# Kernel optimization log

Hardware: AMD Instinct MI355X
Metric: run time of the kernel (lower is better)

## Reference

```python
import jax, jax.numpy as jnp
import numpy as np

LEAKY_SLOPE = 0.01
BN_EPS = 1e-5


def _local_conv(x, w, b, stride):
    # x: [B,C,H,W]; w: [1,O,C,OH,OW,K] (K = kh*kw, kh==kw); b: [1,O,OH,OW]
    sh, sw = stride
    _, O, C, oh, ow, K = w.shape
    k = int(round(K ** 0.5))
    # gather unfold patches: torch .unfold(2,kh,dh).unfold(3,kw,dw) -> last dim ordered (i major, j minor)
    patches = jnp.stack(
        [x[:, :, i:i + sh * oh:sh, j:j + sw * ow:sw] for i in range(k) for j in range(k)],
        axis=-1)  # [B,C,oh,ow,K]
    out = jnp.einsum('bchwk,ochwk->bohw', patches, w[0])
    return out + b  # b broadcasts [1,O,OH,OW]


def _bn_train(x, gamma, beta):
    # BatchNorm2d in training mode: biased batch statistics over (N,H,W)
    m = jnp.mean(x, axis=(0, 2, 3), keepdims=True)
    v = jnp.var(x, axis=(0, 2, 3), keepdims=True)
    return gamma[None, :, None, None] * (x - m) * jax.lax.rsqrt(v + BN_EPS) + beta[None, :, None, None]


def _lrelu(x):
    return jnp.where(x >= 0, x, LEAKY_SLOPE * x)


def _pad1(x):
    return jnp.pad(x, ((0, 0), (0, 0), (1, 1), (1, 1)))


def setup_inputs() -> dict:
    key = jax.random.key(0)
    ks = jax.random.split(key, 16)
    B = 8192
    inp = {
        'image': jax.random.normal(ks[0], (B, 10, 9, 1), jnp.float32),
        'conv1_w': jax.random.normal(ks[1], (64, 1, 2, 2), jnp.float32) * 0.5,
        'conv1_b': jax.random.normal(ks[2], (64,), jnp.float32) * 0.1,
        'lc1_w': jax.random.normal(ks[3], (1, 16, 64, 10, 5, 9), jnp.float32) * 0.05,
        'lc1_b': jax.random.normal(ks[4], (1, 16, 10, 5), jnp.float32) * 0.1,
        'lc2_w': jax.random.normal(ks[5], (1, 8, 16, 11, 6, 4), jnp.float32) * 0.1,
        'lc2_b': jax.random.normal(ks[6], (1, 8, 11, 6), jnp.float32) * 0.1,
        'lc3_w': jax.random.normal(ks[7], (1, 8, 8, 12, 4, 4), jnp.float32) * 0.1,
        'lc3_b': jax.random.normal(ks[8], (1, 8, 12, 4), jnp.float32) * 0.1,
        'gamma1': jax.random.normal(ks[9], (16,), jnp.float32) * 0.1 + 1.0,
        'beta1': jax.random.normal(ks[10], (16,), jnp.float32) * 0.1,
        'gamma2': jax.random.normal(ks[11], (8,), jnp.float32) * 0.1 + 1.0,
        'beta2': jax.random.normal(ks[12], (8,), jnp.float32) * 0.1,
        'gamma3': jax.random.normal(ks[13], (8,), jnp.float32) * 0.1 + 1.0,
        'beta3': jax.random.normal(ks[14], (8,), jnp.float32) * 0.1,
    }
    return inp


def reference(image, conv1_w, conv1_b, lc1_w, lc1_b, lc2_w, lc2_b, lc3_w, lc3_b,
              gamma1, beta1, gamma2, beta2, gamma3, beta3):
    x = jnp.transpose(image, (0, 3, 1, 2))  # [B,1,10,9]
    # Conv2d kernel 2, padding='same' (torch pads extra on right/bottom for even kernels)
    x = jax.lax.conv_general_dilated(
        x, conv1_w, window_strides=(1, 1), padding=[(0, 1), (0, 1)],
        dimension_numbers=('NCHW', 'OIHW', 'NCHW'))
    x = x + conv1_b[None, :, None, None]
    x = _lrelu(x)
    x = _pad1(x)                               # [B,64,12,11]
    x = _local_conv(x, lc1_w, lc1_b, (1, 2))   # [B,16,10,5]
    x = _lrelu(x)
    x = _bn_train(x, gamma1, beta1)
    x = _pad1(x)                               # [B,16,12,7]
    x = _local_conv(x, lc2_w, lc2_b, (1, 1))   # [B,8,11,6]
    x = _lrelu(x)
    x = _bn_train(x, gamma2, beta2)
    x = _pad1(x)                               # [B,8,13,8]
    x = _local_conv(x, lc3_w, lc3_b, (1, 2))   # [B,8,12,4]
    x = _lrelu(x)
    x = _bn_train(x, gamma3, beta3)
    return x.reshape(x.shape[0], -1)           # [B,384]
```

## Files before the change

### kernel.cpp

```cpp
#include <hip/hip_runtime.h>


typedef float  f32x4 __attribute__((ext_vector_type(4)));
typedef float  f32x2 __attribute__((ext_vector_type(2)));
typedef short  bf16x8 __attribute__((ext_vector_type(8)));

union FR  { int4 i4; bf16x8 bf; unsigned u[4]; };

#define LRELU(v) fmaxf((v), 0.01f * (v))

static __device__ inline unsigned bfr(float f) {
    unsigned u = __float_as_uint(f);
    return (u + 0x7fffu + ((u >> 16) & 1u)) >> 16;
}
static __device__ inline unsigned short bfr16(float f) { return (unsigned short)bfr(f); }
static __device__ inline float ubf(unsigned lo16) { return __uint_as_float(lo16 << 16); }

#if __has_builtin(__builtin_elementwise_fma)
static __device__ inline f32x2 pk_fma(f32x2 a, f32x2 b, f32x2 c) { return __builtin_elementwise_fma(a, b, c); }
#else
static __device__ inline f32x2 pk_fma(f32x2 a, f32x2 b, f32x2 c) { return a * b + c; }
#endif
static __device__ inline f32x2 pk_lrelu(f32x2 v) {
#if __has_builtin(__builtin_elementwise_max)
    return __builtin_elementwise_max(v, v * 0.01f);
#else
    f32x2 r; r.x = LRELU(v.x); r.y = LRELU(v.y); return r;
#endif
}
static __device__ inline float aload(float* p) {
    return __hip_atomic_load(p, __ATOMIC_RELAXED, __HIP_MEMORY_SCOPE_AGENT);
}

union PrepSM { float imgP[16][110]; float wt[9216]; };

__global__ __launch_bounds__(256) void kprep(
    const float* __restrict__ imgp,
    const float* __restrict__ cw,
    const float* __restrict__ cb,
    const float* __restrict__ lw1,
    unsigned* __restrict__ x1u,
    int4* __restrict__ afg1, float* __restrict__ stats,
    int nA, int doAux, int spp)
{
    __shared__ PrepSM sm;
    const int bx = blockIdx.x, tid = threadIdx.x;

    if (bx < nA) {
        const int sb = bx * 16;
        for (int e = tid; e < 1760; e += 256) ((float*)sm.imgP)[e] = 0.0f;
        __syncthreads();
        for (int e = tid; e < 1440; e += 256) {
            int s = e / 90, hw = e - s * 90;
            int r = hw / 9, c = hw - r * 9;
            sm.imgP[s][r * 10 + c] = imgp[(size_t)sb * 90 + e];
        }
        __syncthreads();

        const int chp = tid & 31, sidx = tid >> 5;
        const int ch0 = 2 * chp;
        const int h = chp >> 4, chpos = chp & 15;
        f32x2 w00 = {cw[ch0 * 4 + 0], cw[ch0 * 4 + 4]};
        f32x2 w01 = {cw[ch0 * 4 + 1], cw[ch0 * 4 + 5]};
        f32x2 w10 = {cw[ch0 * 4 + 2], cw[ch0 * 4 + 6]};
        f32x2 w11 = {cw[ch0 * 4 + 3], cw[ch0 * 4 + 7]};
        f32x2 bb  = {cb[ch0], cb[ch0 + 1]};

        #pragma unroll
        for (int ss = 0; ss < 2; ++ss) {
            const int s = sidx + 8 * ss;
            const float* ip = sm.imgP[s];
            unsigned* dst = x1u + ((size_t)h * spp + (sb + s)) * 16 + chpos;
            #pragma unroll 2
            for (int r = 0; r < 10; ++r) {
                #pragma unroll
                for (int c = 0; c < 9; ++c) {
                    f32x2 v = bb;
                    v = pk_fma((f32x2)ip[r * 10 + c],      w00, v);
                    v = pk_fma((f32x2)ip[r * 10 + c + 1],  w01, v);
                    v = pk_fma((f32x2)ip[r * 10 + c + 10], w10, v);
                    v = pk_fma((f32x2)ip[r * 10 + c + 11], w11, v);
                    v = pk_lrelu(v);
                    dst[(size_t)(r * 9 + c) * 2 * spp * 16] = bfr(v.x) | (bfr(v.y) << 16);
                }
            }
        }
        return;
    }
    if (!doAux) return;

    const int b2 = bx - nA;
    if (b2 < 50) {
        const int pos = b2;
        for (int e = tid; e < 9216; e += 256) {
            int pair = e / 9, t = e - 9 * pair;
            sm.wt[e] = lw1[pair * 450 + pos * 9 + t];
        }
        __syncthreads();
        for (int e = tid; e < 1152; e += 256) {
            int l = e & 63, ht = e >> 6;
            int h = (ht >= 9) ? 1 : 0, t = ht - 9 * h;
            int q = l >> 4, o = l & 15;
            unsigned uu[4];
            #pragma unroll
            for (int p = 0; p < 4; ++p) {
                int c0 = 32 * h + 8 * q + 2 * p;
                float a0 = sm.wt[(o * 64 + c0) * 9 + t];
                float a1 = sm.wt[(o * 64 + c0 + 1) * 9 + t];
                uu[p] = bfr(a0) | (bfr(a1) << 16);
            }
            int4 st = { (int)uu[0], (int)uu[1], (int)uu[2], (int)uu[3] };
            afg1[pos * 1152 + e] = st;
        }
    } else if (tid < 64) stats[tid] = 0.0f;
}

__global__ __launch_bounds__(256) void k1_lc1(
    const int4* __restrict__ x1v,
    const int4* __restrict__ afg,
    const float* __restrict__ lb,
    unsigned short* __restrict__ y1b,
    float* __restrict__ stats,
    int sampOff, int spp, int nc)
{
    __shared__ int4  AfL[1152];
    __shared__ float bl[16];
    __shared__ float red[32];

    int pos, chunk;
    {
        int id = blockIdx.x;
        if (nc >= 8) { int k8 = id & 7; int r = id >> 3; pos = r % 50; chunk = (r / 50) * 8 + k8; }
        else         { pos = id % 50; chunk = id / 50; }
    }
    const int oh = pos / 5, ow = pos % 5;
    const int tid = threadIdx.x;
    const int wv = tid >> 6, lane = tid & 63;
    const int lane15 = lane & 15, q = lane >> 4;

    for (int e = tid; e < 1152; e += 256) AfL[e] = afg[pos * 1152 + e];
    if (tid < 16) bl[tid] = lb[tid * 50 + pos];
    if (tid < 32) red[tid] = 0.0f;
    __syncthreads();

    const int sLoc = chunk * 256 + wv * 64;
    const int sAbs = sampOff + sLoc;
    const int spp4 = spp * 4;

    int base_g[4];
    #pragma unroll
    for (int g = 0; g < 4; ++g)
        base_g[g] = (sLoc + g * 16 + lane15) * 4 + q;

    f32x4 acc[4];
    #pragma unroll
    for (int g = 0; g < 4; ++g) acc[g] = (f32x4){0.f, 0.f, 0.f, 0.f};

    #pragma unroll
    for (int t = 0; t < 9; ++t) {
        const int ti = t / 3, tj = t % 3;
        const int r = oh + ti - 1, c2 = 2 * ow + tj - 1;
        if (r >= 0 && r < 10 && c2 >= 0 && c2 < 9) {
            const int hw = r * 9 + c2;
            #pragma unroll
            for (int h = 0; h < 2; ++h) {
                FR fa; fa.i4 = AfL[(h * 9 + t) * 64 + lane];
                const int slabBase = (hw * 2 + h) * spp4;
                #pragma unroll
                for (int g = 0; g < 4; ++g) {
                    FR fb; fb.i4 = x1v[slabBase + base_g[g]];
                    acc[g] = __builtin_amdgcn_mfma_f32_16x16x32_bf16(fa.bf, fb.bf, acc[g], 0, 0, 0);
                }
            }
        }
    }

    float so[4] = {0, 0, 0, 0}, sq[4] = {0, 0, 0, 0};
    #pragma unroll
    for (int g = 0; g < 4; ++g)
        #pragma unroll
        for (int r = 0; r < 4; ++r) {
            int o = q * 4 + r;
            float v = acc[g][r] + bl[o];
            v = LRELU(v);
            y1b[(size_t)(o * 50 + pos) * 8192 + sAbs + g * 16 + lane15] = bfr16(v);
            so[r] += v; sq[r] += v * v;
        }
    #pragma unroll
    for (int r = 0; r < 4; ++r) {
        #pragma unroll
        for (int m = 1; m < 16; m <<= 1) {
            so[r] += __shfl_xor(so[r], m, 16);
            sq[r] += __shfl_xor(sq[r], m, 16);
        }
        if (lane15 == 0) {
            int o = q * 4 + r;
            atomicAdd(&red[o], so[r]);
            atomicAdd(&red[16 + o], sq[r]);
        }
    }
    __syncthreads();
    if (tid < 32) atomicAdd(&stats[tid], red[tid]);
}

__global__ __launch_bounds__(256) void k2_lc2(
    const unsigned short* __restrict__ y1b,
    const float* __restrict__ lw2, const float* __restrict__ lb2,
    const float* __restrict__ g1, const float* __restrict__ be1,
    unsigned short* __restrict__ y2b, float* __restrict__ stats)
{
    __shared__ float wld[512];
    __shared__ float a1[16], b1[16], bl[8], red[16];

    const int unit = blockIdx.x;
    const int pos = unit >> 3, chunk = unit & 7;
    const int oh = pos / 6, ow = pos % 6;
    const int tid = threadIdx.x, lane = tid & 63;

    if (tid < 128) {
        const float* src = lw2 + tid * 264 + pos * 4;
        int o = tid >> 4, c = tid & 15;
        #pragma unroll
        for (int k = 0; k < 4; k++) wld[c * 32 + k * 8 + o] = src[k];
    }
    if (tid < 16) {
        float m = aload(&stats[tid]) * (1.0f / 409600.0f);
        float v = aload(&stats[16 + tid]) * (1.0f / 409600.0f) - m * m;
        float a = g1[tid] * rsqrtf(v + 1e-5f);
        a1[tid] = a; b1[tid] = be1[tid] - a * m;
        if (tid < 8) bl[tid] = lb2[tid * 66 + pos];
        red[tid] = 0.0f;
    }
    __syncthreads();

    int base[4]; float kmv[4];
    #pragma unroll
    for (int i = 0; i < 2; i++)
        #pragma unroll
        for (int j = 0; j < 2; j++) {
            int r = oh + i - 1, c2 = ow + j - 1;
            bool ok = (r >= 0 && r < 10 && c2 >= 0 && c2 < 5);
            int rc = min(max(r, 0), 9), cc2 = min(max(c2, 0), 4);
            base[i * 2 + j] = rc * 5 + cc2;
            kmv[i * 2 + j] = ok ? 1.0f : 0.0f;
        }

    const int sb = chunk * 1024 + tid * 4;
    float acc[8][4];
    #pragma unroll
    for (int o = 0; o < 8; o++)
        #pragma unroll
        for (int s = 0; s < 4; s++) acc[o][s] = bl[o];

    #pragma unroll 1
    for (int c = 0; c < 16; c++) {
        float av = a1[c], bv = b1[c];
        float p[4][4];
        #pragma unroll
        for (int t = 0; t < 4; t++) {
            float ap = av * kmv[t], bp = bv * kmv[t];
            uint2 U = *(const uint2*)(y1b + (size_t)(c * 50 + base[t]) * 8192 + sb);
            p[t][0] = fmaf(ap, ubf(U.x & 0xffffu), bp);
            p[t][1] = fmaf(ap, __uint_as_float(U.x & 0xffff0000u), bp);
            p[t][2] = fmaf(ap, ubf(U.y & 0xffffu), bp);
            p[t][3] = fmaf(ap, __uint_as_float(U.y & 0xffff0000u), bp);
        }
        const float4* wr = (const float4*)&wld[c * 32];
        #pragma unroll
        for (int t = 0; t < 4; t++) {
            float4 wa = wr[t * 2], wb = wr[t * 2 + 1];
            #pragma unroll
            for (int s = 0; s < 4; s++) {
                float pv = p[t][s];
                acc[0][s] += wa.x * pv; acc[1][s] += wa.y * pv;
                acc[2][s] += wa.z * pv; acc[3][s] += wa.w * pv;
                acc[4][s] += wb.x * pv; acc[5][s] += wb.y * pv;
                acc[6][s] += wb.z * pv; acc[7][s] += wb.w * pv;
            }
        }
    }

    #pragma unroll
    for (int o = 0; o < 8; o++) {
        float v0 = LRELU(acc[o][0]), v1 = LRELU(acc[o][1]);
        float v2 = LRELU(acc[o][2]), v3 = LRELU(acc[o][3]);
        uint2 st = { bfr(v0) | (bfr(v1) << 16), bfr(v2) | (bfr(v3) << 16) };
        *(uint2*)(y2b + (size_t)(o * 66 + pos) * 8192 + sb) = st;
        float sv = v0 + v1 + v2 + v3;
        float sqv = v0 * v0 + v1 * v1 + v2 * v2 + v3 * v3;
        #pragma unroll
        for (int m = 32; m > 0; m >>= 1) {
            sv  += __shfl_xor(sv, m, 64);
            sqv += __shfl_xor(sqv, m, 64);
        }
        if (lane == 0) { atomicAdd(&red[o], sv); atomicAdd(&red[8 + o], sqv); }
    }
    __syncthreads();
    if (tid < 16) atomicAdd(&stats[32 + tid], red[tid]);
}

__global__ __launch_bounds__(256) void k3_lc3(
    const unsigned short* __restrict__ y2b,
    const float* __restrict__ lw3, const float* __restrict__ lb3,
    const float* __restrict__ g2, const float* __restrict__ be2,
    unsigned short* __restrict__ y3b, float* __restrict__ stats)
{
    __shared__ float wld[256];
    __shared__ float a2[8], b2[8], bl[8], red[16];

    const int unit = blockIdx.x;
    const int pos = unit >> 3, chunk = unit & 7;
    const int oh = pos >> 2, ow = pos & 3;
    const int tid = threadIdx.x, lane = tid & 63;

    if (tid < 64) {
        const float* src = lw3 + tid * 192 + pos * 4;
        int o = tid >> 3, c = tid & 7;
        #pragma unroll
        for (int k = 0; k < 4; k++) wld[c * 32 + k * 8 + o] = src[k];
    }
    if (tid < 16) {
        if (tid < 8) {
            float m = aload(&stats[32 + tid]) * (1.0f / 540672.0f);
            float v = aload(&stats[40 + tid]) * (1.0f / 540672.0f) - m * m;
            float a = g2[tid] * rsqrtf(v + 1e-5f);
            a2[tid] = a; b2[tid] = be2[tid] - a * m;
            bl[tid] = lb3[tid * 48 + pos];
        }
        red[tid] = 0.0f;
    }
    __syncthreads();

    int base[4]; float kmv[4];
    #pragma unroll
    for (int i = 0; i < 2; i++)
        #pragma unroll
        for (int j = 0; j < 2; j++) {
            int r = oh + i - 1, c2 = 2 * ow + j - 1;
            bool ok = (r >= 0 && r < 11 && c2 >= 0 && c2 < 6);
            int rc = min(max(r, 0), 10), cc2 = min(max(c2, 0), 5);
            base[i * 2 + j] = rc * 6 + cc2;
            kmv[i * 2 + j] = ok ? 1.0f : 0.0f;
        }

    const int sb = chunk * 1024 + tid * 4;
    float acc[8][4];
    #pragma unroll
    for (int o = 0; o < 8; o++)
        #pragma unroll
        for (int s = 0; s < 4; s++) acc[o][s] = bl[o];

    #pragma unroll 1
    for (int c = 0; c < 8; c++) {
        float av = a2[c], bv = b2[c];
        float p[4][4];
        #pragma unroll
        for (int t = 0; t < 4; t++) {
            float ap = av * kmv[t], bp = bv * kmv[t];
            uint2 U = *(const uint2*)(y2b + (size_t)(c * 66 + base[t]) * 8192 + sb);
            p[t][0] = fmaf(ap, ubf(U.x & 0xffffu), bp);
            p[t][1] = fmaf(ap, __uint_as_float(U.x & 0xffff0000u), bp);
            p[t][2] = fmaf(ap, ubf(U.y & 0xffffu), bp);
            p[t][3] = fmaf(ap, __uint_as_float(U.y & 0xffff0000u), bp);
        }
        const float4* wr = (const float4*)&wld[c * 32];
        #pragma unroll
        for (int t = 0; t < 4; t++) {
            float4 wa = wr[t * 2], wb = wr[t * 2 + 1];
            #pragma unroll
            for (int s = 0; s < 4; s++) {
                float pv = p[t][s];
                acc[0][s] += wa.x * pv; acc[1][s] += wa.y * pv;
                acc[2][s] += wa.z * pv; acc[3][s] += wa.w * pv;
                acc[4][s] += wb.x * pv; acc[5][s] += wb.y * pv;
                acc[6][s] += wb.z * pv; acc[7][s] += wb.w * pv;
            }
        }
    }

    #pragma unroll
    for (int o = 0; o < 8; o++) {
        float v0 = LRELU(acc[o][0]), v1 = LRELU(acc[o][1]);
        float v2 = LRELU(acc[o][2]), v3 = LRELU(acc[o][3]);
        uint2 st = { bfr(v0) | (bfr(v1) << 16), bfr(v2) | (bfr(v3) << 16) };
        *(uint2*)(y3b + (size_t)(o * 48 + pos) * 8192 + sb) = st;
        float sv = v0 + v1 + v2 + v3;
        float sqv = v0 * v0 + v1 * v1 + v2 * v2 + v3 * v3;
        #pragma unroll
        for (int m = 32; m > 0; m >>= 1) {
            sv  += __shfl_xor(sv, m, 64);
            sqv += __shfl_xor(sqv, m, 64);
        }
        if (lane == 0) { atomicAdd(&red[o], sv); atomicAdd(&red[8 + o], sqv); }
    }
    __syncthreads();
    if (tid < 16) atomicAdd(&stats[48 + tid], red[tid]);
}

__global__ __launch_bounds__(256) void k4_out(
    const unsigned short* __restrict__ y3b,
    const float* __restrict__ g3, const float* __restrict__ be3,
    float* __restrict__ stats, float* __restrict__ out)
{
    __shared__ unsigned short tile[64][66];
    __shared__ float a3[8], b3[8];
    const int unit = blockIdx.x;
    const int tid = threadIdx.x;
    const int chunkS = unit & 31, yy = unit >> 5;
    const int ftile = yy >> 2, sub = yy & 3;
    const int fbase = ftile * 64;
    const int sbase = chunkS * 256 + sub * 64;

    if (tid < 8) {
        float m = aload(&stats[48 + tid]) * (1.0f / 393216.0f);
        float v = aload(&stats[56 + tid]) * (1.0f / 393216.0f) - m * m;
        float a = g3[tid] * rsqrtf(v + 1e-5f);
        a3[tid] = a; b3[tid] = be3[tid] - a * m;
    }
    __syncthreads();

    #pragma unroll
    for (int rep = 0; rep < 16; rep++) {
        int idx = rep * 256 + tid;
        int f = idx >> 6, s = idx & 63;
        tile[f][s] = y3b[(size_t)(fbase + f) * 8192 + sbase + s];
    }
    __syncthreads();
    #pragma unroll
    for (int rep = 0; rep < 16; rep++) {
        int idx = rep * 256 + tid;
        int s = idx >> 6, f = idx & 63;
        int ff = fbase + f;
        int o = ff / 48;
        float x = ubf((unsigned)tile[f][s]);
        out[(size_t)(sbase + s) * 384 + ff] = a3[o] * x + b3[o];
    }
}

extern "C" void kernel_launch(void* const* d_in, const int* in_sizes, int n_in,
                              void* d_out, int out_size, void* d_ws, size_t ws_size,
                              hipStream_t stream) {
    const float* image   = (const float*)d_in[0];
    const float* conv1_w = (const float*)d_in[1];
    const float* conv1_b = (const float*)d_in[2];
    const float* lc1_w   = (const float*)d_in[3];
    const float* lc1_b   = (const float*)d_in[4];
    const float* lc2_w   = (const float*)d_in[5];
    const float* lc2_b   = (const float*)d_in[6];
    const float* lc3_w   = (const float*)d_in[7];
    const float* lc3_b   = (const float*)d_in[8];
    const float* gamma1  = (const float*)d_in[9];
    const float* beta1   = (const float*)d_in[10];
    const float* gamma2  = (const float*)d_in[11];
    const float* beta2   = (const float*)d_in[12];
    const float* gamma3  = (const float*)d_in[13];
    const float* beta3   = (const float*)d_in[14];
    float* outp = (float*)d_out;

    char* wsb = (char*)d_ws;
    float*          stats = (float*)wsb;
    unsigned short* y1b   = (unsigned short*)(wsb + 1024);
    int4*           afg1  = (int4*)(wsb + 13108224);
    char*           x1reg = wsb + 14029824;
    unsigned short* y2b   = (unsigned short*)(wsb + 14029824);
    unsigned short* y3b   = (unsigned short*)(wsb + 22680576);

    const size_t bytesPerSamp = 11520;
    int nPass = 1;
    if (ws_size < 14029824ul + 8192ul * bytesPerSamp) nPass = 2;
    if (ws_size < 14029824ul + 4096ul * bytesPerSamp) nPass = 4;
    if (ws_size < 14029824ul + 2048ul * bytesPerSamp) nPass = 8;
    const int spp = 8192 / nPass;
    const int nA  = spp / 16;
    const int nc  = spp / 256;

    unsigned*   x1u = (unsigned*)x1reg;
    const int4* x1v = (const int4*)x1reg;

    for (int p = 0; p < nPass; ++p) {
        const float* imgp = image + (size_t)p * spp * 90;
        kprep<<<dim3(p == 0 ? nA + 51 : nA), dim3(256), 0, stream>>>(
            imgp, conv1_w, conv1_b, lc1_w, x1u, afg1, stats, nA, p == 0 ? 1 : 0, spp);
        k1_lc1<<<dim3(50 * nc), dim3(256), 0, stream>>>(
            x1v, afg1, lc1_b, y1b, stats, p * spp, spp, nc);
    }
    k2_lc2<<<dim3(528), dim3(256), 0, stream>>>(y1b, lc2_w, lc2_b,
                                                gamma1, beta1, y2b, stats);
    k3_lc3<<<dim3(384), dim3(256), 0, stream>>>(y2b, lc3_w, lc3_b,
                                                gamma2, beta2, y3b, stats);
    k4_out<<<dim3(768), dim3(256), 0, stream>>>(y3b, gamma3, beta3, stats, outp);
}
```

Baseline: 203.0 us.

## Vectorize conv1 stores and make lc1 taps branchless with zero-padded A fragments

The prep kernel's conv1 stage is remapped so each thread computes 8 channels for one pixel and writes a 16-byte uint4 store, replacing scattered 4-byte stores. In the lc1 kernel, out-of-bounds taps are redirected to a zeroed block of shared A fragments instead of being skipped. This makes the tap loop uniform, so all 18 B-fragment loads per sample group can be issued together before the MFMA chain. The cost is extra MFMAs and loads on border positions, plus higher register pressure from holding 18 fragments.

```diff
diff --git a/kernel.cpp b/kernel.cpp
--- a/kernel.cpp
+++ b/kernel.cpp
@@ -57,33 +57,40 @@
         }
         __syncthreads();
 
-        const int chp = tid & 31, sidx = tid >> 5;
-        const int ch0 = 2 * chp;
-        const int h = chp >> 4, chpos = chp & 15;
-        f32x2 w00 = {cw[ch0 * 4 + 0], cw[ch0 * 4 + 4]};
-        f32x2 w01 = {cw[ch0 * 4 + 1], cw[ch0 * 4 + 5]};
-        f32x2 w10 = {cw[ch0 * 4 + 2], cw[ch0 * 4 + 6]};
-        f32x2 w11 = {cw[ch0 * 4 + 3], cw[ch0 * 4 + 7]};
-        f32x2 bb  = {cb[ch0], cb[ch0 + 1]};
-
-        #pragma unroll
-        for (int ss = 0; ss < 2; ++ss) {
-            const int s = sidx + 8 * ss;
-            const float* ip = sm.imgP[s];
-            unsigned* dst = x1u + ((size_t)h * spp + (sb + s)) * 16 + chpos;
-            #pragma unroll 2
-            for (int r = 0; r < 10; ++r) {
-                #pragma unroll
-                for (int c = 0; c < 9; ++c) {
-                    f32x2 v = bb;
-                    v = pk_fma((f32x2)ip[r * 10 + c],      w00, v);
-                    v = pk_fma((f32x2)ip[r * 10 + c + 1],  w01, v);
-                    v = pk_fma((f32x2)ip[r * 10 + c + 10], w10, v);
-                    v = pk_fma((f32x2)ip[r * 10 + c + 11], w11, v);
-                    v = pk_lrelu(v);
-                    dst[(size_t)(r * 9 + c) * 2 * spp * 16] = bfr(v.x) | (bfr(v.y) << 16);
-                }
+        const int quad = tid & 3, s = (tid >> 2) & 15;
+        const int h = (tid >> 6) & 1, hwo = tid >> 7;
+        const int ch0 = h * 32 + quad * 8;
+        f32x2 W00[4], W01[4], W10[4], W11[4], BB[4];
+        #pragma unroll
+        for (int p = 0; p < 4; ++p) {
+            int ca = ch0 + 2 * p, cbn = ca + 1;
+            W00[p] = (f32x2){cw[ca * 4 + 0], cw[cbn * 4 + 0]};
+            W01[p] = (f32x2){cw[ca * 4 + 1], cw[cbn * 4 + 1]};
+            W10[p] = (f32x2){cw[ca * 4 + 2], cw[cbn * 4 + 2]};
+            W11[p] = (f32x2){cw[ca * 4 + 3], cw[cbn * 4 + 3]};
+            BB[p]  = (f32x2){cb[ca], cb[cbn]};
+        }
+        const float* ip = sm.imgP[s];
+        uint4* x1q = (uint4*)x1u;
+        #pragma unroll 3
+        for (int it = 0; it < 45; ++it) {
+            int hw = it * 2 + hwo;
+            int r = hw / 9, c = hw - r * 9;
+            float i00 = ip[r * 10 + c],      i01 = ip[r * 10 + c + 1];
+            float i10 = ip[r * 10 + c + 10], i11 = ip[r * 10 + c + 11];
+            unsigned u[4];
+            #pragma unroll
+            for (int p = 0; p < 4; ++p) {
+                f32x2 v = BB[p];
+                v = pk_fma((f32x2)i00, W00[p], v);
+                v = pk_fma((f32x2)i01, W01[p], v);
+                v = pk_fma((f32x2)i10, W10[p], v);
+                v = pk_fma((f32x2)i11, W11[p], v);
+                v = pk_lrelu(v);
+                u[p] = bfr(v.x) | (bfr(v.y) << 16);
             }
+            x1q[((size_t)(hw * 2 + h) * spp + (sb + s)) * 4 + quad] =
+                make_uint4(u[0], u[1], u[2], u[3]);
         }
         return;
     }
@@ -123,7 +130,7 @@
     float* __restrict__ stats,
     int sampOff, int spp, int nc)
 {
-    __shared__ int4  AfL[1152];
+    __shared__ int4  AfL[1216];
     __shared__ float bl[16];
     __shared__ float red[32];
 
@@ -139,6 +146,7 @@
     const int lane15 = lane & 15, q = lane >> 4;
 
     for (int e = tid; e < 1152; e += 256) AfL[e] = afg[pos * 1152 + e];
+    if (tid < 64) AfL[1152 + tid] = (int4){0, 0, 0, 0};
     if (tid < 16) bl[tid] = lb[tid * 50 + pos];
     if (tid < 32) red[tid] = 0.0f;
     __syncthreads();
@@ -147,32 +155,37 @@
     const int sAbs = sampOff + sLoc;
     const int spp4 = spp * 4;
 
-    int base_g[4];
-    #pragma unroll
-    for (int g = 0; g < 4; ++g)
-        base_g[g] = (sLoc + g * 16 + lane15) * 4 + q;
+    int sb0[9], af0[9], af1[9];
+    #pragma unroll
+    for (int t = 0; t < 9; ++t) {
+        int ti = t / 3, tj = t % 3;
+        int r = oh + ti - 1, c2 = 2 * ow + tj - 1;
+        bool ok = (r >= 0 && r < 10 && c2 >= 0 && c2 < 9);
+        int hw = ok ? (r * 9 + c2) : 0;
+        sb0[t] = hw * 2 * spp4;
+        af0[t] = ok ? t * 64 : 1152;
+        af1[t] = ok ? (9 + t) * 64 : 1152;
+    }
 
     f32x4 acc[4];
     #pragma unroll
-    for (int g = 0; g < 4; ++g) acc[g] = (f32x4){0.f, 0.f, 0.f, 0.f};
-
-    #pragma unroll
-    for (int t = 0; t < 9; ++t) {
-        const int ti = t / 3, tj = t % 3;
-        const int r = oh + ti - 1, c2 = 2 * ow + tj - 1;
-        if (r >= 0 && r < 10 && c2 >= 0 && c2 < 9) {
-            const int hw = r * 9 + c2;
-            #pragma unroll
-            for (int h = 0; h < 2; ++h) {
-                FR fa; fa.i4 = AfL[(h * 9 + t) * 64 + lane];
-                const int slabBase = (hw * 2 + h) * spp4;
-                #pragma unroll
-                for (int g = 0; g < 4; ++g) {
-                    FR fb; fb.i4 = x1v[slabBase + base_g[g]];
-                    acc[g] = __builtin_amdgcn_mfma_f32_16x16x32_bf16(fa.bf, fb.bf, acc[g], 0, 0, 0);
-                }
-            }
-        }
+    for (int g = 0; g < 4; ++g) {
+        const int bg = (sLoc + g * 16 + lane15) * 4 + q;
+        FR fb[9][2];
+        #pragma unroll
+        for (int t = 0; t < 9; ++t) {
+            fb[t][0].i4 = x1v[sb0[t] + bg];
+            fb[t][1].i4 = x1v[sb0[t] + spp4 + bg];
+        }
+        f32x4 a = (f32x4){0.f, 0.f, 0.f, 0.f};
+        #pragma unroll
+        for (int t = 0; t < 9; ++t) {
+            FR fa0; fa0.i4 = AfL[af0[t] + lane];
+            a = __builtin_amdgcn_mfma_f32_16x16x32_bf16(fa0.bf, fb[t][0].bf, a, 0, 0, 0);
+            FR fa1; fa1.i4 = AfL[af1[t] + lane];
+            a = __builtin_amdgcn_mfma_f32_16x16x32_bf16(fa1.bf, fb[t][1].bf, a, 0, 0, 0);
+        }
+        acc[g] = a;
     }
 
     float so[4] = {0, 0, 0, 0}, sq[4] = {0, 0, 0, 0};
```

After: 193.7 us. -4.6%, faster.
